# Performance work log

Hardware: AMD Instinct MI355X
Metric: run time of the kernel (lower is better)

The kernel has to match this reference:

```python
import jax, jax.numpy as jnp
import numpy as np

VOCAB = 50000
D = 512          # in_feat == word_embedding_dim
B = 4096
S = 128
NUM_LABELS = 3


def setup_inputs() -> dict:
    key = jax.random.key(0)
    ks = jax.random.split(key, 16)
    ids_a = jax.random.randint(ks[0], (B, S), 0, VOCAB, dtype=jnp.int32)
    ids_b = jax.random.randint(ks[1], (B, S), 0, VOCAB, dtype=jnp.int32)
    mask_a = jax.random.randint(ks[2], (B, S), 0, 2) > 0
    mask_b = jax.random.randint(ks[3], (B, S), 0, 2) > 0
    s = 0.02
    W_emb = jax.random.normal(ks[4], (VOCAB, D), jnp.float32) * s
    W_emb = W_emb.at[0].set(0.0)  # padding_idx=0
    enc_w1 = jax.random.normal(ks[5], (D, D), jnp.float32) * s
    enc_b1 = jnp.zeros((D,), jnp.float32)
    enc_w2 = jax.random.normal(ks[6], (D, D), jnp.float32) * s
    enc_b2 = jnp.zeros((D,), jnp.float32)
    cls_w1 = jax.random.normal(ks[7], (2 * D, D), jnp.float32) * s
    cls_b1 = jnp.zeros((D,), jnp.float32)
    cls_w2 = jax.random.normal(ks[8], (D, NUM_LABELS), jnp.float32) * s
    cls_b2 = jnp.zeros((NUM_LABELS,), jnp.float32)
    return {
        "text_a_inputs_id": ids_a, "text_b_inputs_id": ids_b,
        "text_a_attention_mask": mask_a, "text_b_attention_mask": mask_b,
        "W_emb": W_emb,
        "enc_w1": enc_w1, "enc_b1": enc_b1, "enc_w2": enc_w2, "enc_b2": enc_b2,
        "cls_w1": cls_w1, "cls_b1": cls_b1, "cls_w2": cls_w2, "cls_b2": cls_b2,
    }


def _encode(ids, mask, W_emb, w1, b1, w2, b2):
    # embedding gather [B,S,D], fused masked sum-pool -> [B,D]
    emb = W_emb[ids]
    pooled = jnp.einsum("bsd,bs->bd", emb, mask.astype(emb.dtype))
    x = jnp.tanh(pooled @ w1 + b1)
    x = jnp.tanh(x @ w2 + b2)  # dropout is identity in eval
    return x


def reference(text_a_inputs_id, text_b_inputs_id, text_a_attention_mask,
              text_b_attention_mask, W_emb, enc_w1, enc_b1, enc_w2, enc_b2,
              cls_w1, cls_b1, cls_w2, cls_b2):
    va = _encode(text_a_inputs_id, text_a_attention_mask, W_emb, enc_w1, enc_b1, enc_w2, enc_b2)
    vb = _encode(text_b_inputs_id, text_b_attention_mask, W_emb, enc_w1, enc_b1, enc_w2, enc_b2)
    pooled = jnp.concatenate([va, vb], axis=-1)  # [B, 2D]
    h = jnp.tanh(pooled @ cls_w1 + cls_b1)
    logits = h @ cls_w2 + cls_b2  # [B, num_labels]
    return logits
```

## Files before the change

kernel.cpp:

```cpp
#include <hip/hip_runtime.h>


typedef unsigned short u16;
typedef __attribute__((ext_vector_type(8))) short short8;
typedef __attribute__((ext_vector_type(4))) float f32x4;

__device__ __forceinline__ float bfu2f(u16 u) {
    union { unsigned int i; float f; } v;
    v.i = ((unsigned int)u) << 16;
    return v.f;
}

__device__ __forceinline__ u16 f2bfu(float f) {
    union { float f; unsigned int i; } v;
    v.f = f;
    unsigned int x = v.i;
    x += 0x7fffu + ((x >> 16) & 1u);
    return (u16)(x >> 16);
}

__device__ __forceinline__ int detect_wave(const u16* __restrict__ W,
                                           const unsigned int* __restrict__ m,
                                           int lane)
{
    int cnt = 0;
    int w01 = 1, b01 = 1, lo16 = 0;
    #pragma unroll
    for (int j = lane; j < 256; j += 64) {
        u16 u = W[1024 + 2 * j];
        int e = (u >> 7) & 0xFF;
        cnt += (e >= 0x6A && e <= 0x7E) ? 1 : 0;
        unsigned int v = m[j];
        w01 &= (v <= 1u) ? 1 : 0;
        b01 &= ((v & ~0x01010101u) == 0u) ? 1 : 0;
        lo16 |= ((v & 0xFFFFu) == 0x3F80u) ? 1 : 0;
    }
    #pragma unroll
    for (int off = 32; off > 0; off >>= 1) {
        cnt  += __shfl_down(cnt, off);
        w01  &= __shfl_down(w01, off);
        b01  &= __shfl_down(b01, off);
        lo16 |= __shfl_down(lo16, off);
    }
    int mtype;
    if (w01)        mtype = 0;
    else if (b01)   mtype = 1;
    else if (lo16)  mtype = 2;
    else            mtype = 3;
    int fl = ((cnt >= 128) ? 1 : 0) | (mtype << 2);
    return __shfl(fl, 0);
}

__device__ __forceinline__ int mask_nonzero(const void* __restrict__ msk,
                                            int idx, int mtype)
{
    switch (mtype) {
        case 0:  return ((const int*)msk)[idx] != 0;
        case 1:  return ((const unsigned char*)msk)[idx] != 0;
        case 2:  return ((const u16*)msk)[idx] != 0;
        default: return ((const unsigned int*)msk)[idx] != 0u;
    }
}

__global__ __launch_bounds__(128) void pool_kernel(
    const int* __restrict__ ids_a, const int* __restrict__ ids_b,
    const void* __restrict__ mask_a, const void* __restrict__ mask_b,
    const void* __restrict__ W, u16* __restrict__ P)
{
    __shared__ int s_ids[128];
    __shared__ int s_cnt;
    __shared__ int s_flags;
    __shared__ float sP[512];
    const int t = threadIdx.x;
    const int w = t >> 6;
    const int lane = t & 63;

    if (t == 0) s_cnt = 0;
    if (t < 64) {
        int fl = detect_wave((const u16*)W, (const unsigned int*)mask_a, t);
        if (t == 0) s_flags = fl;
    }
    __syncthreads();
    const int  flags = s_flags;
    const bool isbf  = (flags & 1) != 0;
    const int  mtype = (flags >> 2) & 3;

    const int row  = blockIdx.x & 4095;
    const int side = blockIdx.x >> 12;
    const int* __restrict__ ids = side ? ids_b : ids_a;
    const void* __restrict__ msk = side ? mask_b : mask_a;

    int id = ids[row * 128 + t];
    int mk = mask_nonzero(msk, row * 128 + t, mtype);
    if (mk) {
        int idx = atomicAdd(&s_cnt, 1);
        s_ids[idx] = id;
    }
    __syncthreads();
    const int cnt = s_cnt;

    float acc[8] = {};
    if (isbf) {
        const u16* Wb = (const u16*)W;
        int j = w;
        for (; j + 6 < cnt; j += 8) {
            union { uint4 v; u16 s[8]; } r0, r1, r2, r3;
            r0.v = *(const uint4*)(Wb + (size_t)s_ids[j + 0] * 512 + lane * 8);
            r1.v = *(const uint4*)(Wb + (size_t)s_ids[j + 2] * 512 + lane * 8);
            r2.v = *(const uint4*)(Wb + (size_t)s_ids[j + 4] * 512 + lane * 8);
            r3.v = *(const uint4*)(Wb + (size_t)s_ids[j + 6] * 512 + lane * 8);
            #pragma unroll
            for (int i = 0; i < 8; ++i)
                acc[i] += bfu2f(r0.s[i]) + bfu2f(r1.s[i]) +
                          bfu2f(r2.s[i]) + bfu2f(r3.s[i]);
        }
        for (; j < cnt; j += 2) {
            union { uint4 v; u16 s[8]; } r;
            r.v = *(const uint4*)(Wb + (size_t)s_ids[j] * 512 + lane * 8);
            #pragma unroll
            for (int i = 0; i < 8; ++i) acc[i] += bfu2f(r.s[i]);
        }
    } else {
        const float* Wf = (const float*)W;
        for (int j = w; j < cnt; j += 2) {
            const float* rp = Wf + (size_t)s_ids[j] * 512 + lane * 8;
            float4 a = *(const float4*)(rp + 0);
            float4 b = *(const float4*)(rp + 4);
            acc[0] += a.x; acc[1] += a.y; acc[2] += a.z; acc[3] += a.w;
            acc[4] += b.x; acc[5] += b.y; acc[6] += b.z; acc[7] += b.w;
        }
    }

    if (w == 0) {
        #pragma unroll
        for (int i = 0; i < 8; ++i) sP[lane * 8 + i] = acc[i];
    }
    __syncthreads();
    if (w == 1) {
        union { uint4 v; u16 s[8]; } o;
        #pragma unroll
        for (int i = 0; i < 8; ++i)
            o.s[i] = f2bfu(acc[i] + sP[lane * 8 + i]);
        *(uint4*)(P + (size_t)blockIdx.x * 512 + lane * 8) = o.v;
    }
}

__global__ __launch_bounds__(256) void gemm_mfma(
    const u16* __restrict__ A, const u16* __restrict__ A2, int K1,
    const void* __restrict__ B, const void* __restrict__ bias,
    u16* __restrict__ C, int N, int K,
    const u16* __restrict__ Wdet, const unsigned int* __restrict__ Mdet)
{
    __shared__ __align__(16) u16 As[128 * 40];
    __shared__ __align__(16) u16 Bs[64 * 40];
    __shared__ int s_flags;

    const int tid  = threadIdx.x;
    const int lane = tid & 63;

    if (tid < 64) {
        int fl = detect_wave(Wdet, Mdet, tid);
        if (tid == 0) s_flags = fl;
    }
    __syncthreads();
    const bool isbf = (s_flags & 1) != 0;

    const int m0 = blockIdx.x * 128;
    const int n0 = blockIdx.y * 64;

    const int wid = tid >> 6;
    const int wm  = (wid & 1) * 64;
    const int wn  = (wid >> 1) * 32;

    const int ar = tid >> 2;
    const int ak = (tid & 3) * 8;
    const int bk = tid >> 3;
    const int jn = tid & 7;
    const int nb = jn * 8;
    const int bofs = (((bk >> 3) + jn) & 3) * 8 + (bk & 7);

    const int lm = lane & 15;
    const int kq = lane >> 4;
    const int kc = kq * 8;

    f32x4 acc[4][2];
    #pragma unroll
    for (int i = 0; i < 4; ++i)
        #pragma unroll
        for (int j = 0; j < 2; ++j)
            acc[i][j] = (f32x4){0.f, 0.f, 0.f, 0.f};

    uint4 ra0, ra1;
    u16 rb[8];

    auto fetch = [&](int k0) {
        const int kg = k0 + ak;
        const u16* Ap0 = (kg < K1) ? (A  + (size_t)(m0 + ar) * 512 + kg)
                                   : (A2 + (size_t)(m0 + ar) * 512 + (kg - K1));
        const u16* Ap1 = (kg < K1) ? (A  + (size_t)(m0 + ar + 64) * 512 + kg)
                                   : (A2 + (size_t)(m0 + ar + 64) * 512 + (kg - K1));
        ra0 = *(const uint4*)Ap0;
        ra1 = *(const uint4*)Ap1;
        if (isbf) {
            union { uint4 v; u16 s[8]; } ub;
            ub.v = *(const uint4*)((const u16*)B + (size_t)(k0 + bk) * N + n0 + nb);
            #pragma unroll
            for (int i = 0; i < 8; ++i) rb[i] = ub.s[i];
        } else {
            const float* Bp = (const float*)B + (size_t)(k0 + bk) * N + n0 + nb;
            float4 b0 = *(const float4*)(Bp + 0);
            float4 b1 = *(const float4*)(Bp + 4);
            rb[0] = f2bfu(b0.x); rb[1] = f2bfu(b0.y); rb[2] = f2bfu(b0.z); rb[3] = f2bfu(b0.w);
            rb[4] = f2bfu(b1.x); rb[5] = f2bfu(b1.y); rb[6] = f2bfu(b1.z); rb[7] = f2bfu(b1.w);
        }
    };

    fetch(0);
    for (int k0 = 0; k0 < K; k0 += 32) {
        if (k0) __syncthreads();
        *(uint4*)&As[ar * 40 + ak]        = ra0;
        *(uint4*)&As[(ar + 64) * 40 + ak] = ra1;
        #pragma unroll
        for (int i = 0; i < 8; ++i)
            Bs[(nb + i) * 40 + bofs] = rb[i];
        __syncthreads();

        if (k0 + 32 < K) fetch(k0 + 32);

        short8 af[4], bf[2];
        #pragma unroll
        for (int i = 0; i < 4; ++i)
            af[i] = *(const short8*)&As[(wm + i * 16 + lm) * 40 + kc];
        #pragma unroll
        for (int j = 0; j < 2; ++j) {
            const int n = wn + j * 16 + lm;
            const int ch = ((kq + (n >> 3)) & 3) * 8;
            bf[j] = *(const short8*)&Bs[n * 40 + ch];
        }
        #pragma unroll
        for (int i = 0; i < 4; ++i)
            #pragma unroll
            for (int j = 0; j < 2; ++j)
                acc[i][j] = __builtin_amdgcn_mfma_f32_16x16x32_bf16(
                    af[i], bf[j], acc[i][j], 0, 0, 0);
    }

    #pragma unroll
    for (int j = 0; j < 2; ++j) {
        const int n = n0 + wn + j * 16 + lm;
        const float bsv = isbf ? bfu2f(((const u16*)bias)[n])
                               : ((const float*)bias)[n];
        #pragma unroll
        for (int i = 0; i < 4; ++i) {
            #pragma unroll
            for (int r = 0; r < 4; ++r) {
                const int m = m0 + wm + i * 16 + kq * 4 + r;
                C[(size_t)m * N + n] = f2bfu(tanhf(acc[i][j][r] + bsv));
            }
        }
    }
}

__global__ __launch_bounds__(64) void logits_kernel(
    const u16* __restrict__ H, const void* __restrict__ W2,
    const void* __restrict__ b2, float* __restrict__ out,
    const u16* __restrict__ Wdet, const unsigned int* __restrict__ Mdet)
{
    const int lane = threadIdx.x;
    const int fl = detect_wave(Wdet, Mdet, lane);
    const bool isbf = (fl & 1) != 0;

    const int m = blockIdx.x;
    union { uint4 v; u16 s[8]; } h;
    h.v = *(const uint4*)(H + (size_t)m * 512 + lane * 8);

    float a0 = 0.f, a1 = 0.f, a2 = 0.f;
    #pragma unroll
    for (int i = 0; i < 8; ++i) {
        const int k = lane * 8 + i;
        float x = bfu2f(h.s[i]);
        float w0, w1, w2;
        if (isbf) {
            const u16* Wb = (const u16*)W2;
            w0 = bfu2f(Wb[k * 3 + 0]); w1 = bfu2f(Wb[k * 3 + 1]); w2 = bfu2f(Wb[k * 3 + 2]);
        } else {
            const float* Wf = (const float*)W2;
            w0 = Wf[k * 3 + 0]; w1 = Wf[k * 3 + 1]; w2 = Wf[k * 3 + 2];
        }
        a0 += x * w0; a1 += x * w1; a2 += x * w2;
    }
    #pragma unroll
    for (int off = 32; off > 0; off >>= 1) {
        a0 += __shfl_down(a0, off);
        a1 += __shfl_down(a1, off);
        a2 += __shfl_down(a2, off);
    }
    if (lane == 0) {
        float b0, b1, b2v;
        if (isbf) {
            const u16* bb = (const u16*)b2;
            b0 = bfu2f(bb[0]); b1 = bfu2f(bb[1]); b2v = bfu2f(bb[2]);
        } else {
            const float* bf = (const float*)b2;
            b0 = bf[0]; b1 = bf[1]; b2v = bf[2];
        }
        out[m * 3 + 0] = a0 + b0;
        out[m * 3 + 1] = a1 + b1;
        out[m * 3 + 2] = a2 + b2v;
    }
}

extern "C" void kernel_launch(void* const* d_in, const int* in_sizes, int n_in,
                              void* d_out, int out_size, void* d_ws, size_t ws_size,
                              hipStream_t stream)
{
    const int* ids_a  = (const int*)d_in[0];
    const int* ids_b  = (const int*)d_in[1];
    const void* mask_a = d_in[2];
    const void* mask_b = d_in[3];
    const void* W_emb  = d_in[4];
    const void* enc_w1 = d_in[5];
    const void* enc_b1 = d_in[6];
    const void* enc_w2 = d_in[7];
    const void* enc_b2 = d_in[8];
    const void* cls_w1 = d_in[9];
    const void* cls_b1 = d_in[10];
    const void* cls_w2 = d_in[11];
    const void* cls_b2 = d_in[12];

    const u16* Wdet = (const u16*)W_emb;
    const unsigned int* Mdet = (const unsigned int*)mask_a;

    u16* buf0 = (u16*)d_ws;
    u16* buf1 = buf0 + (size_t)8192 * 512;

    pool_kernel<<<8192, 128, 0, stream>>>(ids_a, ids_b, mask_a, mask_b, W_emb, buf0);

    gemm_mfma<<<dim3(64, 8), 256, 0, stream>>>(
        buf0, buf0, 512, enc_w1, enc_b1, buf1, 512, 512, Wdet, Mdet);

    gemm_mfma<<<dim3(64, 8), 256, 0, stream>>>(
        buf1, buf1, 512, enc_w2, enc_b2, buf0, 512, 512, Wdet, Mdet);

    gemm_mfma<<<dim3(32, 8), 256, 0, stream>>>(
        buf0, buf0 + (size_t)4096 * 512, 512, cls_w1, cls_b1, buf1, 512, 1024, Wdet, Mdet);

    logits_kernel<<<4096, 64, 0, stream>>>(buf1, cls_w2, cls_b2, (float*)d_out, Wdet, Mdet);
}
```

Baseline: 383.6 us.

## Template GEMM on dtype, use fast tanh, split pooling into two launches

```diff
diff --git a/kernel.cpp b/kernel.cpp
--- a/kernel.cpp
+++ b/kernel.cpp
@@ -17,6 +17,12 @@
     unsigned int x = v.i;
     x += 0x7fffu + ((x >> 16) & 1u);
     return (u16)(x >> 16);
+}
+
+__device__ __forceinline__ float fast_tanh(float x) {
+    float xc = fminf(fmaxf(x, -15.f), 15.f);
+    float e = __builtin_amdgcn_exp2f(xc * 2.885390082f);
+    return (e - 1.f) / (e + 1.f);
 }
 
 __device__ __forceinline__ int detect_wave(const u16* __restrict__ W,
@@ -63,9 +69,9 @@
 }
 
 __global__ __launch_bounds__(128) void pool_kernel(
-    const int* __restrict__ ids_a, const int* __restrict__ ids_b,
-    const void* __restrict__ mask_a, const void* __restrict__ mask_b,
-    const void* __restrict__ W, u16* __restrict__ P)
+    const int* __restrict__ ids, const void* __restrict__ msk,
+    const void* __restrict__ W, u16* __restrict__ P,
+    const unsigned int* __restrict__ Mdet)
 {
     __shared__ int s_ids[128];
     __shared__ int s_cnt;
@@ -77,7 +83,7 @@
 
     if (t == 0) s_cnt = 0;
     if (t < 64) {
-        int fl = detect_wave((const u16*)W, (const unsigned int*)mask_a, t);
+        int fl = detect_wave((const u16*)W, Mdet, t);
         if (t == 0) s_flags = fl;
     }
     __syncthreads();
@@ -85,10 +91,7 @@
     const bool isbf  = (flags & 1) != 0;
     const int  mtype = (flags >> 2) & 3;
 
-    const int row  = blockIdx.x & 4095;
-    const int side = blockIdx.x >> 12;
-    const int* __restrict__ ids = side ? ids_b : ids_a;
-    const void* __restrict__ msk = side ? mask_b : mask_a;
+    const int row = blockIdx.x;
 
     int id = ids[row * 128 + t];
     int mk = mask_nonzero(msk, row * 128 + t, mtype);
@@ -141,47 +144,36 @@
         #pragma unroll
         for (int i = 0; i < 8; ++i)
             o.s[i] = f2bfu(acc[i] + sP[lane * 8 + i]);
-        *(uint4*)(P + (size_t)blockIdx.x * 512 + lane * 8) = o.v;
-    }
-}
-
-__global__ __launch_bounds__(256) void gemm_mfma(
+        *(uint4*)(P + (size_t)row * 512 + lane * 8) = o.v;
+    }
+}
+
+template<bool ISBF>
+__device__ __forceinline__ void gemm_body(
     const u16* __restrict__ A, const u16* __restrict__ A2, int K1,
-    const void* __restrict__ B, const void* __restrict__ bias,
+    const void* __restrict__ Bv, const void* __restrict__ biasv,
     u16* __restrict__ C, int N, int K,
-    const u16* __restrict__ Wdet, const unsigned int* __restrict__ Mdet)
-{
-    __shared__ __align__(16) u16 As[128 * 40];
-    __shared__ __align__(16) u16 Bs[64 * 40];
-    __shared__ int s_flags;
-
+    u16* __restrict__ As, u16* __restrict__ Bs)
+{
     const int tid  = threadIdx.x;
     const int lane = tid & 63;
-
-    if (tid < 64) {
-        int fl = detect_wave(Wdet, Mdet, tid);
-        if (tid == 0) s_flags = fl;
-    }
-    __syncthreads();
-    const bool isbf = (s_flags & 1) != 0;
-
-    const int m0 = blockIdx.x * 128;
-    const int n0 = blockIdx.y * 64;
-
     const int wid = tid >> 6;
     const int wm  = (wid & 1) * 64;
     const int wn  = (wid >> 1) * 32;
-
     const int ar = tid >> 2;
     const int ak = (tid & 3) * 8;
     const int bk = tid >> 3;
     const int jn = tid & 7;
     const int nb = jn * 8;
     const int bofs = (((bk >> 3) + jn) & 3) * 8 + (bk & 7);
-
     const int lm = lane & 15;
     const int kq = lane >> 4;
     const int kc = kq * 8;
+    const int m0 = blockIdx.x * 128;
+    const int n0 = blockIdx.y * 64;
+
+    const u16*   Bb = (const u16*)Bv;
+    const float* Bf = (const float*)Bv;
 
     f32x4 acc[4][2];
     #pragma unroll
@@ -191,41 +183,46 @@
             acc[i][j] = (f32x4){0.f, 0.f, 0.f, 0.f};
 
     uint4 ra0, ra1;
-    u16 rb[8];
-
-    auto fetch = [&](int k0) {
-        const int kg = k0 + ak;
-        const u16* Ap0 = (kg < K1) ? (A  + (size_t)(m0 + ar) * 512 + kg)
-                                   : (A2 + (size_t)(m0 + ar) * 512 + (kg - K1));
-        const u16* Ap1 = (kg < K1) ? (A  + (size_t)(m0 + ar + 64) * 512 + kg)
-                                   : (A2 + (size_t)(m0 + ar + 64) * 512 + (kg - K1));
-        ra0 = *(const uint4*)Ap0;
-        ra1 = *(const uint4*)Ap1;
-        if (isbf) {
-            union { uint4 v; u16 s[8]; } ub;
-            ub.v = *(const uint4*)((const u16*)B + (size_t)(k0 + bk) * N + n0 + nb);
-            #pragma unroll
-            for (int i = 0; i < 8; ++i) rb[i] = ub.s[i];
-        } else {
-            const float* Bp = (const float*)B + (size_t)(k0 + bk) * N + n0 + nb;
-            float4 b0 = *(const float4*)(Bp + 0);
-            float4 b1 = *(const float4*)(Bp + 4);
-            rb[0] = f2bfu(b0.x); rb[1] = f2bfu(b0.y); rb[2] = f2bfu(b0.z); rb[3] = f2bfu(b0.w);
-            rb[4] = f2bfu(b1.x); rb[5] = f2bfu(b1.y); rb[6] = f2bfu(b1.z); rb[7] = f2bfu(b1.w);
-        }
-    };
-
-    fetch(0);
+    uint4 rbb;
+    float4 rf0, rf1;
+
+    #define FETCH(k0)                                                         \
+    {                                                                         \
+        const int kg = (k0) + ak;                                             \
+        const u16* base = (kg < K1) ? (A + kg) : (A2 + (kg - K1));            \
+        ra0 = *(const uint4*)(base + (size_t)(m0 + ar) * 512);                \
+        ra1 = *(const uint4*)(base + (size_t)(m0 + ar + 64) * 512);           \
+        if constexpr (ISBF) {                                                 \
+            rbb = *(const uint4*)(Bb + (size_t)((k0) + bk) * N + n0 + nb);    \
+        } else {                                                              \
+            const float* Bp = Bf + (size_t)((k0) + bk) * N + n0 + nb;         \
+            rf0 = *(const float4*)(Bp + 0);                                   \
+            rf1 = *(const float4*)(Bp + 4);                                   \
+        }                                                                     \
+    }
+
+    FETCH(0)
     for (int k0 = 0; k0 < K; k0 += 32) {
         if (k0) __syncthreads();
         *(uint4*)&As[ar * 40 + ak]        = ra0;
         *(uint4*)&As[(ar + 64) * 40 + ak] = ra1;
+        u16 bvals[8];
+        if constexpr (ISBF) {
+            union { uint4 v; u16 s[8]; } ub; ub.v = rbb;
+            #pragma unroll
+            for (int i = 0; i < 8; ++i) bvals[i] = ub.s[i];
+        } else {
+            bvals[0] = f2bfu(rf0.x); bvals[1] = f2bfu(rf0.y);
+            bvals[2] = f2bfu(rf0.z); bvals[3] = f2bfu(rf0.w);
+            bvals[4] = f2bfu(rf1.x); bvals[5] = f2bfu(rf1.y);
+            bvals[6] = f2bfu(rf1.z); bvals[7] = f2bfu(rf1.w);
+        }
         #pragma unroll
         for (int i = 0; i < 8; ++i)
-            Bs[(nb + i) * 40 + bofs] = rb[i];
+            Bs[(nb + i) * 40 + bofs] = bvals[i];
         __syncthreads();
 
-        if (k0 + 32 < K) fetch(k0 + 32);
+        if (k0 + 32 < K) FETCH(k0 + 32)
 
         short8 af[4], bf[2];
         #pragma unroll
@@ -244,21 +241,41 @@
                 acc[i][j] = __builtin_amdgcn_mfma_f32_16x16x32_bf16(
                     af[i], bf[j], acc[i][j], 0, 0, 0);
     }
+    #undef FETCH
 
     #pragma unroll
     for (int j = 0; j < 2; ++j) {
         const int n = n0 + wn + j * 16 + lm;
-        const float bsv = isbf ? bfu2f(((const u16*)bias)[n])
-                               : ((const float*)bias)[n];
+        const float bsv = ISBF ? bfu2f(((const u16*)biasv)[n])
+                               : ((const float*)biasv)[n];
         #pragma unroll
         for (int i = 0; i < 4; ++i) {
             #pragma unroll
             for (int r = 0; r < 4; ++r) {
                 const int m = m0 + wm + i * 16 + kq * 4 + r;
-                C[(size_t)m * N + n] = f2bfu(tanhf(acc[i][j][r] + bsv));
+                C[(size_t)m * N + n] = f2bfu(fast_tanh(acc[i][j][r] + bsv));
             }
         }
     }
+}
+
+__global__ __launch_bounds__(256, 2) void gemm_mfma(
+    const u16* __restrict__ A, const u16* __restrict__ A2, int K1,
+    const void* __restrict__ B, const void* __restrict__ bias,
+    u16* __restrict__ C, int N, int K,
+    const u16* __restrict__ Wdet, const unsigned int* __restrict__ Mdet)
+{
+    __shared__ __align__(16) u16 As[128 * 40];
+    __shared__ __align__(16) u16 Bs[64 * 40];
+    __shared__ int s_flags;
+
+    if (threadIdx.x < 64) {
+        int fl = detect_wave(Wdet, Mdet, threadIdx.x);
+        if (threadIdx.x == 0) s_flags = fl;
+    }
+    __syncthreads();
+    if (s_flags & 1) gemm_body<true >(A, A2, K1, B, bias, C, N, K, As, Bs);
+    else             gemm_body<false>(A, A2, K1, B, bias, C, N, K, As, Bs);
 }
 
 __global__ __launch_bounds__(64) void logits_kernel(
@@ -334,7 +351,9 @@
     u16* buf0 = (u16*)d_ws;
     u16* buf1 = buf0 + (size_t)8192 * 512;
 
-    pool_kernel<<<8192, 128, 0, stream>>>(ids_a, ids_b, mask_a, mask_b, W_emb, buf0);
+    pool_kernel<<<4096, 128, 0, stream>>>(ids_a, mask_a, W_emb, buf0, Mdet);
+    pool_kernel<<<4096, 128, 0, stream>>>(ids_b, mask_b, W_emb,
+                                          buf0 + (size_t)4096 * 512, Mdet);
 
     gemm_mfma<<<dim3(64, 8), 256, 0, stream>>>(
         buf0, buf0, 512, enc_w1, enc_b1, buf1, 512, 512, Wdet, Mdet);
```

Measured after the change: 376.1 us. About the same (-2.0%).
